# Performance work log

Hardware: AMD Instinct MI355X
Metric: run time of the kernel (lower is better)

Reference implementation:

```python
import jax, jax.numpy as jnp
import numpy as np

N_USERS = 100000
N_ITEMS = 50000
N_NODES = N_USERS + N_ITEMS
EMB_DIM = 128
N_LAYERS = 3
NNZ = 4800000


def setup_inputs() -> dict:
    key = jax.random.key(0)
    k1, k2, k3, k4, k5 = jax.random.split(key, 5)
    user_table = jax.random.normal(k1, (N_USERS, EMB_DIM), dtype=jnp.float32) * 0.005
    item_table = jax.random.normal(k2, (N_ITEMS, EMB_DIM), dtype=jnp.float32) * 0.005
    graph_rows = jax.random.randint(k3, (NNZ,), 0, N_NODES, dtype=jnp.int32)
    graph_cols = jax.random.randint(k4, (NNZ,), 0, N_NODES, dtype=jnp.int32)
    # values of the symmetrically-normalized adjacency are small positives
    graph_vals = jax.random.uniform(k5, (NNZ,), dtype=jnp.float32) * (1.0 / 32.0)
    return {
        "user_table": user_table,
        "item_table": item_table,
        "graph_rows": graph_rows,
        "graph_cols": graph_cols,
        "graph_vals": graph_vals,
    }


def reference(user_table, item_table, graph_rows, graph_cols, graph_vals):
    # LightGCN.get_embeddings: multi-hop SpMM over fixed COO graph + layer mean
    all_emb = jnp.concatenate([user_table, item_table], axis=0)  # [N, d]
    acc = all_emb
    emb = all_emb
    for _ in range(N_LAYERS):
        # sparse.mm(graph, emb): gather source rows, scale by edge value, scatter-add to dest
        gathered = emb[graph_cols] * graph_vals[:, None]          # [nnz, d]
        emb = jax.ops.segment_sum(gathered, graph_rows, num_segments=N_NODES)
        acc = acc + emb
    mean_emb = acc / jnp.float32(N_LAYERS + 1)
    return mean_emb[:N_USERS], mean_emb[N_USERS:]
```

## Files before the change

### kernel.cpp

```cpp
#include <hip/hip_runtime.h>

#define N_USERS 100000
#define N_ITEMS 50000
#define N_NODES 150000
#define EMB_DIM 128

#define NB 147
#define BUCKET_SHIFT 10
#define TILE 16384

#define VAL_SCALE_ENC 524288.0f

#define ENC1 (1.0f / 131072.0f)
#define ENC2 (1.0f / 131072.0f * 0.5f)
#undef ENC2
#define ENC2 (1.0f / 131072.0f)
#define DEC3 (1.0f / 68719476736.0f / 0.5f)
#undef DEC3
#define DEC_E3 (1.0f / 34359738368.0f)
#define DEC_E1 (1.0f / 16384.0f)
#define DEC_E2 (1.0f / 65536.0f)

typedef float f32x2 __attribute__((ext_vector_type(2)));

static __device__ __forceinline__ unsigned int pack_edge(int col, float val) {
    unsigned int q = (unsigned int)fminf(val * VAL_SCALE_ENC + 0.5f, 16383.0f);
    return ((unsigned int)col << 14) | q;
}
static __device__ __forceinline__ int q8(float x) {
    int q = (int)rintf(x);
    return (q < -128 ? -128 : (q > 127 ? 127 : q)) & 0xff;
}
static __device__ __forceinline__ int sx_lo(unsigned int g) { return ((int)(g << 24)) >> 24; }
static __device__ __forceinline__ int sx_hi(unsigned int g) { return ((int)(g << 16)) >> 24; }

__global__ void init_kernel(const float* __restrict__ user,
                            const float* __restrict__ item,
                            unsigned int* __restrict__ e0q) {
    size_t i = (size_t)blockIdx.x * blockDim.x + threadIdx.x;
    const size_t total = (size_t)N_NODES * EMB_DIM / 4;
    if (i >= total) return;
    const size_t user_vecs = (size_t)N_USERS * EMB_DIM / 4;
    float4 v;
    if (i < user_vecs) v = ((const float4*)user)[i];
    else               v = ((const float4*)item)[i - user_vecs];
    unsigned int q0 = q8(v.x * 4096.0f);
    unsigned int q1 = q8(v.y * 4096.0f);
    unsigned int q2 = q8(v.z * 4096.0f);
    unsigned int q3 = q8(v.w * 4096.0f);
    e0q[i] = q0 | (q1 << 8) | (q2 << 16) | (q3 << 24);
}

__global__ void bhist_kernel(const int* __restrict__ rows,
                             int* __restrict__ bsize, int nnz) {
    __shared__ int h[NB];
    for (int t = threadIdx.x; t < NB; t += blockDim.x) h[t] = 0;
    __syncthreads();
    int n4 = nnz >> 2;
    const int4* rows4 = (const int4*)rows;
    for (int i = blockIdx.x * blockDim.x + threadIdx.x; i < n4;
         i += gridDim.x * blockDim.x) {
        int4 r = rows4[i];
        atomicAdd(&h[r.x >> BUCKET_SHIFT], 1);
        atomicAdd(&h[r.y >> BUCKET_SHIFT], 1);
        atomicAdd(&h[r.z >> BUCKET_SHIFT], 1);
        atomicAdd(&h[r.w >> BUCKET_SHIFT], 1);
    }
    if (blockIdx.x == 0 && threadIdx.x < (nnz & 3))
        atomicAdd(&h[rows[(nnz & ~3) + threadIdx.x] >> BUCKET_SHIFT], 1);
    __syncthreads();
    for (int t = threadIdx.x; t < NB; t += blockDim.x)
        if (h[t]) atomicAdd(&bsize[t], h[t]);
}

__global__ void bscan_kernel(const int* __restrict__ bsize,
                             int* __restrict__ bs, int* __restrict__ gcnt,
                             int* __restrict__ row_ptr, int nnz) {
    __shared__ int s[256];
    int t = threadIdx.x;
    int v = (t < NB) ? bsize[t] : 0;
    s[t] = v;
    __syncthreads();
    for (int off = 1; off < 256; off <<= 1) {
        int a = (t >= off) ? s[t - off] : 0;
        __syncthreads();
        s[t] += a;
        __syncthreads();
    }
    if (t < NB) { bs[t] = s[t] - v; gcnt[t] = s[t] - v; }
    if (t == 0) { bs[NB] = nnz; row_ptr[N_NODES] = nnz; }
}

__global__ void partition_kernel(const int* __restrict__ rows,
                                 const int* __restrict__ cols,
                                 const float* __restrict__ vals,
                                 int* __restrict__ gcnt,
                                 uint2* __restrict__ inter, int nnz) {
    __shared__ int hist[NB];
    __shared__ int cur[NB];
    int t = threadIdx.x;
    int base = blockIdx.x * TILE;
    for (int i = t; i < NB; i += blockDim.x) hist[i] = 0;
    __syncthreads();
    #pragma unroll 4
    for (int k = 0; k < TILE / 256; ++k) {
        int idx = base + k * 256 + t;
        if (idx < nnz) atomicAdd(&hist[rows[idx] >> BUCKET_SHIFT], 1);
    }
    __syncthreads();
    for (int i = t; i < NB; i += blockDim.x)
        cur[i] = atomicAdd(&gcnt[i], hist[i]);
    __syncthreads();
    #pragma unroll 4
    for (int k = 0; k < TILE / 256; ++k) {
        int idx = base + k * 256 + t;
        if (idx < nnz) {
            int r = rows[idx];
            int pos = atomicAdd(&cur[r >> BUCKET_SHIFT], 1);
            uint2 rec;
            rec.x = pack_edge(cols[idx], vals[idx]);
            rec.y = (unsigned int)r;
            inter[pos] = rec;
        }
    }
}

__global__ void __launch_bounds__(1024)
bucket_scatter_kernel(const int* __restrict__ bs,
                      const uint2* __restrict__ inter,
                      unsigned int* __restrict__ edges,
                      int* __restrict__ row_ptr) {
    __shared__ int s[1024];
    __shared__ int cur[1024];
    int b = blockIdx.x;
    int t = threadIdx.x;
    int bstart = bs[b], bend = bs[b + 1];
    int rbase = b << BUCKET_SHIFT;
    s[t] = 0;
    __syncthreads();
    for (int j = bstart + t; j < bend; j += 1024)
        atomicAdd(&s[inter[j].y - rbase], 1);
    __syncthreads();
    int myv = s[t];
    for (int off = 1; off < 1024; off <<= 1) {
        int a = (t >= off) ? s[t - off] : 0;
        __syncthreads();
        s[t] += a;
        __syncthreads();
    }
    int excl = bstart + s[t] - myv;
    int row = rbase + t;
    if (row < N_NODES) row_ptr[row] = excl;
    cur[t] = excl;
    __syncthreads();
    for (int j = bstart + t; j < bend; j += 1024) {
        uint2 rec = inter[j];
        int pos = atomicAdd(&cur[rec.y - rbase], 1);
        edges[pos] = rec.x;
    }
}

__global__ void pull_kernel(const int* __restrict__ row_ptr,
                            const unsigned int* __restrict__ edges,
                            const unsigned short* __restrict__ emb_in,
                            unsigned short* __restrict__ emb_out,
                            float enc) {
    int wave = blockIdx.x * (blockDim.x >> 6) + (threadIdx.x >> 6);
    int lane = threadIdx.x & 63;
    if (wave >= N_NODES) return;
    int beg = __builtin_amdgcn_readfirstlane(row_ptr[wave]);
    int end = __builtin_amdgcn_readfirstlane(row_ptr[wave + 1]);

    float ax = 0.f, ay = 0.f, bx = 0.f, by = 0.f;
    float cx = 0.f, cy = 0.f, dx = 0.f, dy = 0.f;
    int j = beg;
    for (; j + 3 < end; j += 4) {
        unsigned int w0 = edges[j + 0];
        unsigned int w1 = edges[j + 1];
        unsigned int w2 = edges[j + 2];
        unsigned int w3 = edges[j + 3];
        unsigned int g0 = emb_in[(size_t)(w0 >> 14) * (EMB_DIM / 2) + lane];
        unsigned int g1 = emb_in[(size_t)(w1 >> 14) * (EMB_DIM / 2) + lane];
        unsigned int g2 = emb_in[(size_t)(w2 >> 14) * (EMB_DIM / 2) + lane];
        unsigned int g3 = emb_in[(size_t)(w3 >> 14) * (EMB_DIM / 2) + lane];
        float v0 = (float)(w0 & 0x3FFFu);
        float v1 = (float)(w1 & 0x3FFFu);
        float v2 = (float)(w2 & 0x3FFFu);
        float v3 = (float)(w3 & 0x3FFFu);
        ax += v0 * (float)sx_lo(g0); ay += v0 * (float)sx_hi(g0);
        bx += v1 * (float)sx_lo(g1); by += v1 * (float)sx_hi(g1);
        cx += v2 * (float)sx_lo(g2); cy += v2 * (float)sx_hi(g2);
        dx += v3 * (float)sx_lo(g3); dy += v3 * (float)sx_hi(g3);
    }
    for (; j < end; ++j) {
        unsigned int w0 = edges[j];
        unsigned int g0 = emb_in[(size_t)(w0 >> 14) * (EMB_DIM / 2) + lane];
        float v0 = (float)(w0 & 0x3FFFu);
        ax += v0 * (float)sx_lo(g0); ay += v0 * (float)sx_hi(g0);
    }
    float sxv = ((ax + bx) + (cx + dx)) * enc;
    float syv = ((ay + by) + (cy + dy)) * enc;
    unsigned int qx = q8(sxv);
    unsigned int qy = q8(syv);
    __builtin_nontemporal_store(
        (unsigned short)(qx | (qy << 8)),
        emb_out + (size_t)wave * (EMB_DIM / 2) + lane);
}

__global__ void pull_final_kernel(const int* __restrict__ row_ptr,
                                  const unsigned int* __restrict__ edges,
                                  const unsigned short* __restrict__ emb_in,
                                  const float* __restrict__ user,
                                  const float* __restrict__ item,
                                  const unsigned short* __restrict__ e1q,
                                  const unsigned short* __restrict__ e2q,
                                  float* __restrict__ out) {
    int wave = blockIdx.x * (blockDim.x >> 6) + (threadIdx.x >> 6);
    int lane = threadIdx.x & 63;
    if (wave >= N_NODES) return;
    int beg = __builtin_amdgcn_readfirstlane(row_ptr[wave]);
    int end = __builtin_amdgcn_readfirstlane(row_ptr[wave + 1]);

    float ax = 0.f, ay = 0.f, bx = 0.f, by = 0.f;
    float cx = 0.f, cy = 0.f, dx = 0.f, dy = 0.f;
    int j = beg;
    for (; j + 3 < end; j += 4) {
        unsigned int w0 = edges[j + 0];
        unsigned int w1 = edges[j + 1];
        unsigned int w2 = edges[j + 2];
        unsigned int w3 = edges[j + 3];
        unsigned int g0 = emb_in[(size_t)(w0 >> 14) * (EMB_DIM / 2) + lane];
        unsigned int g1 = emb_in[(size_t)(w1 >> 14) * (EMB_DIM / 2) + lane];
        unsigned int g2 = emb_in[(size_t)(w2 >> 14) * (EMB_DIM / 2) + lane];
        unsigned int g3 = emb_in[(size_t)(w3 >> 14) * (EMB_DIM / 2) + lane];
        float v0 = (float)(w0 & 0x3FFFu);
        float v1 = (float)(w1 & 0x3FFFu);
        float v2 = (float)(w2 & 0x3FFFu);
        float v3 = (float)(w3 & 0x3FFFu);
        ax += v0 * (float)sx_lo(g0); ay += v0 * (float)sx_hi(g0);
        bx += v1 * (float)sx_lo(g1); by += v1 * (float)sx_hi(g1);
        cx += v2 * (float)sx_lo(g2); cy += v2 * (float)sx_hi(g2);
        dx += v3 * (float)sx_lo(g3); dy += v3 * (float)sx_hi(g3);
    }
    for (; j < end; ++j) {
        unsigned int w0 = edges[j];
        unsigned int g0 = emb_in[(size_t)(w0 >> 14) * (EMB_DIM / 2) + lane];
        float v0 = (float)(w0 & 0x3FFFu);
        ax += v0 * (float)sx_lo(g0); ay += v0 * (float)sx_hi(g0);
    }
    float s3x = ((ax + bx) + (cx + dx)) * DEC_E3;
    float s3y = ((ay + by) + (cy + dy)) * DEC_E3;

    const float2* e0p = (wave < N_USERS)
        ? (const float2*)(user + (size_t)wave * EMB_DIM)
        : (const float2*)(item + (size_t)(wave - N_USERS) * EMB_DIM);
    float2 v0f = e0p[lane];
    unsigned int w1 = e1q[(size_t)wave * (EMB_DIM / 2) + lane];
    unsigned int w2 = e2q[(size_t)wave * (EMB_DIM / 2) + lane];
    float e1x = (float)sx_lo(w1) * DEC_E1, e1y = (float)sx_hi(w1) * DEC_E1;
    float e2x = (float)sx_lo(w2) * DEC_E2, e2y = (float)sx_hi(w2) * DEC_E2;
    f32x2 r;
    r.x = (v0f.x + e1x + e2x + s3x) * 0.25f;
    r.y = (v0f.y + e1y + e2y + s3y) * 0.25f;
    __builtin_nontemporal_store(r, (f32x2*)(out + (size_t)wave * EMB_DIM) + lane);
}

extern "C" void kernel_launch(void* const* d_in, const int* in_sizes, int n_in,
                              void* d_out, int out_size, void* d_ws, size_t ws_size,
                              hipStream_t stream) {
    const float* user = (const float*)d_in[0];
    const float* item = (const float*)d_in[1];
    const int*   rows = (const int*)d_in[2];
    const int*   cols = (const int*)d_in[3];
    const float* vals = (const float*)d_in[4];
    const int    nnz  = in_sizes[2];

    float* out = (float*)d_out;

    const size_t emb_half = (size_t)N_NODES * EMB_DIM / 2;
    unsigned short* e0q = (unsigned short*)d_ws;
    unsigned short* e1q = e0q + emb_half;
    unsigned short* e2q = e1q + emb_half;
    uint2*          inter = (uint2*)(e2q + emb_half);
    unsigned int*   edges = (unsigned int*)(inter + nnz);
    int* row_ptr = (int*)(edges + nnz);
    int* bsize   = row_ptr + N_NODES + 2;
    int* bs      = bsize + NB;
    int* gcnt    = bs + NB + 2;

    const size_t vec_total = (size_t)N_NODES * EMB_DIM / 4;
    const int    vec_blocks = (int)((vec_total + 255) / 256);
    const int    part_blocks = (nnz + TILE - 1) / TILE;

    (void)hipMemsetAsync(bsize, 0, NB * sizeof(int), stream);
    bhist_kernel<<<1024, 256, 0, stream>>>(rows, bsize, nnz);
    bscan_kernel<<<1, 256, 0, stream>>>(bsize, bs, gcnt, row_ptr, nnz);
    partition_kernel<<<part_blocks, 256, 0, stream>>>(rows, cols, vals, gcnt, inter, nnz);
    bucket_scatter_kernel<<<NB, 1024, 0, stream>>>(bs, inter, edges, row_ptr);

    init_kernel<<<vec_blocks, 256, 0, stream>>>(user, item, (unsigned int*)e0q);

    const int pull_blocks = (N_NODES + 3) / 4;
    pull_kernel<<<pull_blocks, 256, 0, stream>>>(row_ptr, edges, e0q, e1q, ENC1);
    pull_kernel<<<pull_blocks, 256, 0, stream>>>(row_ptr, edges, e1q, e2q, ENC2);
    pull_final_kernel<<<pull_blocks, 256, 0, stream>>>(row_ptr, edges, e2q,
                                                       user, item, e1q, e2q, out);
}
```

Measured before the change: 557.6 us.

## Gather 4 int8 dims per lane with half-wave edge split and integer accumulation

The pull kernels now have each lane load a 32-bit word holding four int8 embedding dims instead of a 16-bit pair. The two half-waves process different edges, and their partial sums are combined with a cross-half shuffle at the end. Accumulation switches from float FMAs to integer multiply-adds, and edge words are read with nontemporal loads. This halves the gather instruction count per edge and uses wider memory transactions, at the cost of a shuffle reduction and idle half-wave lanes during the store.

Result: slower. 746.3 us (+33.8%).

```diff
diff --git a/kernel.cpp b/kernel.cpp
--- a/kernel.cpp
+++ b/kernel.cpp
@@ -12,16 +12,12 @@
 #define VAL_SCALE_ENC 524288.0f
 
 #define ENC1 (1.0f / 131072.0f)
-#define ENC2 (1.0f / 131072.0f * 0.5f)
-#undef ENC2
 #define ENC2 (1.0f / 131072.0f)
-#define DEC3 (1.0f / 68719476736.0f / 0.5f)
-#undef DEC3
 #define DEC_E3 (1.0f / 34359738368.0f)
 #define DEC_E1 (1.0f / 16384.0f)
 #define DEC_E2 (1.0f / 65536.0f)
 
-typedef float f32x2 __attribute__((ext_vector_type(2)));
+typedef float f32x4 __attribute__((ext_vector_type(4)));
 
 static __device__ __forceinline__ unsigned int pack_edge(int col, float val) {
     unsigned int q = (unsigned int)fminf(val * VAL_SCALE_ENC + 0.5f, 16383.0f);
@@ -31,8 +27,9 @@
     int q = (int)rintf(x);
     return (q < -128 ? -128 : (q > 127 ? 127 : q)) & 0xff;
 }
-static __device__ __forceinline__ int sx_lo(unsigned int g) { return ((int)(g << 24)) >> 24; }
-static __device__ __forceinline__ int sx_hi(unsigned int g) { return ((int)(g << 16)) >> 24; }
+static __device__ __forceinline__ int sxb(unsigned int g, int k) {
+    return ((int)(g << (24 - 8 * k))) >> 24;
+}
 
 __global__ void init_kernel(const float* __restrict__ user,
                             const float* __restrict__ item,
@@ -162,107 +159,131 @@
 
 __global__ void pull_kernel(const int* __restrict__ row_ptr,
                             const unsigned int* __restrict__ edges,
-                            const unsigned short* __restrict__ emb_in,
-                            unsigned short* __restrict__ emb_out,
+                            const unsigned int* __restrict__ emb_in,
+                            unsigned int* __restrict__ emb_out,
                             float enc) {
     int wave = blockIdx.x * (blockDim.x >> 6) + (threadIdx.x >> 6);
     int lane = threadIdx.x & 63;
+    int half = lane >> 5;
+    int sub  = lane & 31;
     if (wave >= N_NODES) return;
     int beg = __builtin_amdgcn_readfirstlane(row_ptr[wave]);
     int end = __builtin_amdgcn_readfirstlane(row_ptr[wave + 1]);
 
-    float ax = 0.f, ay = 0.f, bx = 0.f, by = 0.f;
-    float cx = 0.f, cy = 0.f, dx = 0.f, dy = 0.f;
+    int a0 = 0, a1 = 0, a2 = 0, a3 = 0;
+    int b0 = 0, b1 = 0, b2 = 0, b3 = 0;
     int j = beg;
     for (; j + 3 < end; j += 4) {
-        unsigned int w0 = edges[j + 0];
-        unsigned int w1 = edges[j + 1];
-        unsigned int w2 = edges[j + 2];
-        unsigned int w3 = edges[j + 3];
-        unsigned int g0 = emb_in[(size_t)(w0 >> 14) * (EMB_DIM / 2) + lane];
-        unsigned int g1 = emb_in[(size_t)(w1 >> 14) * (EMB_DIM / 2) + lane];
-        unsigned int g2 = emb_in[(size_t)(w2 >> 14) * (EMB_DIM / 2) + lane];
-        unsigned int g3 = emb_in[(size_t)(w3 >> 14) * (EMB_DIM / 2) + lane];
-        float v0 = (float)(w0 & 0x3FFFu);
-        float v1 = (float)(w1 & 0x3FFFu);
-        float v2 = (float)(w2 & 0x3FFFu);
-        float v3 = (float)(w3 & 0x3FFFu);
-        ax += v0 * (float)sx_lo(g0); ay += v0 * (float)sx_hi(g0);
-        bx += v1 * (float)sx_lo(g1); by += v1 * (float)sx_hi(g1);
-        cx += v2 * (float)sx_lo(g2); cy += v2 * (float)sx_hi(g2);
-        dx += v3 * (float)sx_lo(g3); dy += v3 * (float)sx_hi(g3);
-    }
-    for (; j < end; ++j) {
-        unsigned int w0 = edges[j];
-        unsigned int g0 = emb_in[(size_t)(w0 >> 14) * (EMB_DIM / 2) + lane];
-        float v0 = (float)(w0 & 0x3FFFu);
-        ax += v0 * (float)sx_lo(g0); ay += v0 * (float)sx_hi(g0);
-    }
-    float sxv = ((ax + bx) + (cx + dx)) * enc;
-    float syv = ((ay + by) + (cy + dy)) * enc;
-    unsigned int qx = q8(sxv);
-    unsigned int qy = q8(syv);
-    __builtin_nontemporal_store(
-        (unsigned short)(qx | (qy << 8)),
-        emb_out + (size_t)wave * (EMB_DIM / 2) + lane);
+        unsigned int wA = __builtin_nontemporal_load(edges + j + half);
+        unsigned int wB = __builtin_nontemporal_load(edges + j + 2 + half);
+        unsigned int gA = emb_in[(size_t)(wA >> 14) * (EMB_DIM / 4) + sub];
+        unsigned int gB = emb_in[(size_t)(wB >> 14) * (EMB_DIM / 4) + sub];
+        int vA = (int)(wA & 0x3FFFu);
+        int vB = (int)(wB & 0x3FFFu);
+        a0 += vA * sxb(gA, 0); a1 += vA * sxb(gA, 1);
+        a2 += vA * sxb(gA, 2); a3 += vA * sxb(gA, 3);
+        b0 += vB * sxb(gB, 0); b1 += vB * sxb(gB, 1);
+        b2 += vB * sxb(gB, 2); b3 += vB * sxb(gB, 3);
+    }
+    for (; j + 1 < end; j += 2) {
+        unsigned int wA = __builtin_nontemporal_load(edges + j + half);
+        unsigned int gA = emb_in[(size_t)(wA >> 14) * (EMB_DIM / 4) + sub];
+        int vA = (int)(wA & 0x3FFFu);
+        a0 += vA * sxb(gA, 0); a1 += vA * sxb(gA, 1);
+        a2 += vA * sxb(gA, 2); a3 += vA * sxb(gA, 3);
+    }
+    if (j < end) {
+        unsigned int wA = __builtin_nontemporal_load(edges + j);
+        unsigned int gA = emb_in[(size_t)(wA >> 14) * (EMB_DIM / 4) + sub];
+        int vA = (half == 0) ? (int)(wA & 0x3FFFu) : 0;
+        a0 += vA * sxb(gA, 0); a1 += vA * sxb(gA, 1);
+        a2 += vA * sxb(gA, 2); a3 += vA * sxb(gA, 3);
+    }
+    a0 += b0; a1 += b1; a2 += b2; a3 += b3;
+    a0 += __shfl_xor(a0, 32, 64);
+    a1 += __shfl_xor(a1, 32, 64);
+    a2 += __shfl_xor(a2, 32, 64);
+    a3 += __shfl_xor(a3, 32, 64);
+
+    if (half == 0) {
+        unsigned int q = (unsigned int)q8((float)a0 * enc)
+                       | ((unsigned int)q8((float)a1 * enc) << 8)
+                       | ((unsigned int)q8((float)a2 * enc) << 16)
+                       | ((unsigned int)q8((float)a3 * enc) << 24);
+        __builtin_nontemporal_store(q, emb_out + (size_t)wave * (EMB_DIM / 4) + sub);
+    }
 }
 
 __global__ void pull_final_kernel(const int* __restrict__ row_ptr,
                                   const unsigned int* __restrict__ edges,
-                                  const unsigned short* __restrict__ emb_in,
+                                  const unsigned int* __restrict__ emb_in,
                                   const float* __restrict__ user,
                                   const float* __restrict__ item,
-                                  const unsigned short* __restrict__ e1q,
-                                  const unsigned short* __restrict__ e2q,
+                                  const unsigned int* __restrict__ e1q,
+                                  const unsigned int* __restrict__ e2q,
                                   float* __restrict__ out) {
     int wave = blockIdx.x * (blockDim.x >> 6) + (threadIdx.x >> 6);
     int lane = threadIdx.x & 63;
+    int half = lane >> 5;
+    int sub  = lane & 31;
     if (wave >= N_NODES) return;
     int beg = __builtin_amdgcn_readfirstlane(row_ptr[wave]);
     int end = __builtin_amdgcn_readfirstlane(row_ptr[wave + 1]);
 
-    float ax = 0.f, ay = 0.f, bx = 0.f, by = 0.f;
-    float cx = 0.f, cy = 0.f, dx = 0.f, dy = 0.f;
+    int a0 = 0, a1 = 0, a2 = 0, a3 = 0;
+    int b0 = 0, b1 = 0, b2 = 0, b3 = 0;
     int j = beg;
     for (; j + 3 < end; j += 4) {
-        unsigned int w0 = edges[j + 0];
-        unsigned int w1 = edges[j + 1];
-        unsigned int w2 = edges[j + 2];
-        unsigned int w3 = edges[j + 3];
-        unsigned int g0 = emb_in[(size_t)(w0 >> 14) * (EMB_DIM / 2) + lane];
-        unsigned int g1 = emb_in[(size_t)(w1 >> 14) * (EMB_DIM / 2) + lane];
-        unsigned int g2 = emb_in[(size_t)(w2 >> 14) * (EMB_DIM / 2) + lane];
-        unsigned int g3 = emb_in[(size_t)(w3 >> 14) * (EMB_DIM / 2) + lane];
-        float v0 = (float)(w0 & 0x3FFFu);
-        float v1 = (float)(w1 & 0x3FFFu);
-        float v2 = (float)(w2 & 0x3FFFu);
-        float v3 = (float)(w3 & 0x3FFFu);
-        ax += v0 * (float)sx_lo(g0); ay += v0 * (float)sx_hi(g0);
-        bx += v1 * (float)sx_lo(g1); by += v1 * (float)sx_hi(g1);
-        cx += v2 * (float)sx_lo(g2); cy += v2 * (float)sx_hi(g2);
-        dx += v3 * (float)sx_lo(g3); dy += v3 * (float)sx_hi(g3);
-    }
-    for (; j < end; ++j) {
-        unsigned int w0 = edges[j];
-        unsigned int g0 = emb_in[(size_t)(w0 >> 14) * (EMB_DIM / 2) + lane];
-        float v0 = (float)(w0 & 0x3FFFu);
-        ax += v0 * (float)sx_lo(g0); ay += v0 * (float)sx_hi(g0);
-    }
-    float s3x = ((ax + bx) + (cx + dx)) * DEC_E3;
-    float s3y = ((ay + by) + (cy + dy)) * DEC_E3;
-
-    const float2* e0p = (wave < N_USERS)
-        ? (const float2*)(user + (size_t)wave * EMB_DIM)
-        : (const float2*)(item + (size_t)(wave - N_USERS) * EMB_DIM);
-    float2 v0f = e0p[lane];
-    unsigned int w1 = e1q[(size_t)wave * (EMB_DIM / 2) + lane];
-    unsigned int w2 = e2q[(size_t)wave * (EMB_DIM / 2) + lane];
-    float e1x = (float)sx_lo(w1) * DEC_E1, e1y = (float)sx_hi(w1) * DEC_E1;
-    float e2x = (float)sx_lo(w2) * DEC_E2, e2y = (float)sx_hi(w2) * DEC_E2;
-    f32x2 r;
-    r.x = (v0f.x + e1x + e2x + s3x) * 0.25f;
-    r.y = (v0f.y + e1y + e2y + s3y) * 0.25f;
-    __builtin_nontemporal_store(r, (f32x2*)(out + (size_t)wave * EMB_DIM) + lane);
+        unsigned int wA = __builtin_nontemporal_load(edges + j + half);
+        unsigned int wB = __builtin_nontemporal_load(edges + j + 2 + half);
+        unsigned int gA = emb_in[(size_t)(wA >> 14) * (EMB_DIM / 4) + sub];
+        unsigned int gB = emb_in[(size_t)(wB >> 14) * (EMB_DIM / 4) + sub];
+        int vA = (int)(wA & 0x3FFFu);
+        int vB = (int)(wB & 0x3FFFu);
+        a0 += vA * sxb(gA, 0); a1 += vA * sxb(gA, 1);
+        a2 += vA * sxb(gA, 2); a3 += vA * sxb(gA, 3);
+        b0 += vB * sxb(gB, 0); b1 += vB * sxb(gB, 1);
+        b2 += vB * sxb(gB, 2); b3 += vB * sxb(gB, 3);
+    }
+    for (; j + 1 < end; j += 2) {
+        unsigned int wA = __builtin_nontemporal_load(edges + j + half);
+        unsigned int gA = emb_in[(size_t)(wA >> 14) * (EMB_DIM / 4) + sub];
+        int vA = (int)(wA & 0x3FFFu);
+        a0 += vA * sxb(gA, 0); a1 += vA * sxb(gA, 1);
+        a2 += vA * sxb(gA, 2); a3 += vA * sxb(gA, 3);
+    }
+    if (j < end) {
+        unsigned int wA = __builtin_nontemporal_load(edges + j);
+        unsigned int gA = emb_in[(size_t)(wA >> 14) * (EMB_DIM / 4) + sub];
+        int vA = (half == 0) ? (int)(wA & 0x3FFFu) : 0;
+        a0 += vA * sxb(gA, 0); a1 += vA * sxb(gA, 1);
+        a2 += vA * sxb(gA, 2); a3 += vA * sxb(gA, 3);
+    }
+    a0 += b0; a1 += b1; a2 += b2; a3 += b3;
+    a0 += __shfl_xor(a0, 32, 64);
+    a1 += __shfl_xor(a1, 32, 64);
+    a2 += __shfl_xor(a2, 32, 64);
+    a3 += __shfl_xor(a3, 32, 64);
+
+    if (half == 0) {
+        float s0 = (float)a0 * DEC_E3;
+        float s1 = (float)a1 * DEC_E3;
+        float s2 = (float)a2 * DEC_E3;
+        float s3 = (float)a3 * DEC_E3;
+        const float4* e0p = (wave < N_USERS)
+            ? (const float4*)user + (size_t)wave * (EMB_DIM / 4)
+            : (const float4*)item + (size_t)(wave - N_USERS) * (EMB_DIM / 4);
+        float4 v0 = e0p[sub];
+        unsigned int w1 = e1q[(size_t)wave * (EMB_DIM / 4) + sub];
+        unsigned int w2 = e2q[(size_t)wave * (EMB_DIM / 4) + sub];
+        f32x4 r;
+        r.x = (v0.x + (float)sxb(w1, 0) * DEC_E1 + (float)sxb(w2, 0) * DEC_E2 + s0) * 0.25f;
+        r.y = (v0.y + (float)sxb(w1, 1) * DEC_E1 + (float)sxb(w2, 1) * DEC_E2 + s1) * 0.25f;
+        r.z = (v0.z + (float)sxb(w1, 2) * DEC_E1 + (float)sxb(w2, 2) * DEC_E2 + s2) * 0.25f;
+        r.w = (v0.w + (float)sxb(w1, 3) * DEC_E1 + (float)sxb(w2, 3) * DEC_E2 + s3) * 0.25f;
+        __builtin_nontemporal_store(
+            r, (f32x4*)(out + (size_t)wave * EMB_DIM) + sub);
+    }
 }
 
 extern "C" void kernel_launch(void* const* d_in, const int* in_sizes, int n_in,
@@ -277,12 +298,12 @@
 
     float* out = (float*)d_out;
 
-    const size_t emb_half = (size_t)N_NODES * EMB_DIM / 2;
-    unsigned short* e0q = (unsigned short*)d_ws;
-    unsigned short* e1q = e0q + emb_half;
-    unsigned short* e2q = e1q + emb_half;
-    uint2*          inter = (uint2*)(e2q + emb_half);
-    unsigned int*   edges = (unsigned int*)(inter + nnz);
+    const size_t emb_dw = (size_t)N_NODES * EMB_DIM / 4;
+    unsigned int* e0q = (unsigned int*)d_ws;
+    unsigned int* e1q = e0q + emb_dw;
+    unsigned int* e2q = e1q + emb_dw;
+    uint2*        inter = (uint2*)(e2q + emb_dw);
+    unsigned int* edges = (unsigned int*)(inter + nnz);
     int* row_ptr = (int*)(edges + nnz);
     int* bsize   = row_ptr + N_NODES + 2;
     int* bs      = bsize + NB;
@@ -298,7 +319,7 @@
     partition_kernel<<<part_blocks, 256, 0, stream>>>(rows, cols, vals, gcnt, inter, nnz);
     bucket_scatter_kernel<<<NB, 1024, 0, stream>>>(bs, inter, edges, row_ptr);
 
-    init_kernel<<<vec_blocks, 256, 0, stream>>>(user, item, (unsigned int*)e0q);
+    init_kernel<<<vec_blocks, 256, 0, stream>>>(user, item, e0q);
 
     const int pull_blocks = (N_NODES + 3) / 4;
     pull_kernel<<<pull_blocks, 256, 0, stream>>>(row_ptr, edges, e0q, e1q, ENC1);
```
